# Kernel tuning notes

Measured on AMD Instinct MI355X. Metric: run time of the kernel, lower is better.

Reference implementation:

```python
import jax, jax.numpy as jnp
import numpy as np

P, H, T, B = 16, 24, 168, 4096


def _lstm(x, W_ih, W_hh, b_ih, b_hh):
    # x: [B, T, F]; PyTorch gate order i, f, g, o; returns all hidden states [B, T, H]
    Bsz = x.shape[0]
    Hd = W_hh.shape[1]
    # batch the input GEMM over all timesteps
    xg = jnp.einsum('btf,gf->btg', x, W_ih) + b_ih + b_hh  # [B, T, 4H]

    def step(carry, xt):
        h, c = carry
        g = xt + h @ W_hh.T  # [B, 4H]
        i, f, gg, o = jnp.split(g, 4, axis=-1)
        c = jax.nn.sigmoid(f) * c + jax.nn.sigmoid(i) * jnp.tanh(gg)
        h = jax.nn.sigmoid(o) * jnp.tanh(c)
        return (h, c), h

    h0 = jnp.zeros((Bsz, Hd), x.dtype)
    _, hs = jax.lax.scan(step, (h0, h0), jnp.swapaxes(xg, 0, 1))
    return jnp.swapaxes(hs, 0, 1)  # [B, T, H]


def setup_inputs() -> dict:
    key = jax.random.key(0)
    ks = jax.random.split(key, 14)
    s1 = 1.0 / np.sqrt(H)
    u = lambda k, shape: jax.random.uniform(k, shape, jnp.float32, -s1, s1)
    return {
        'x': jax.random.normal(ks[0], (B, T, P), jnp.float32),
        'W_ih1': u(ks[1], (4 * H, P)), 'W_hh1': u(ks[2], (4 * H, H)),
        'b_ih1': u(ks[3], (4 * H,)), 'b_hh1': u(ks[4], (4 * H,)),
        'W_ih2': u(ks[5], (4 * H, H)), 'W_hh2': u(ks[6], (4 * H, H)),
        'b_ih2': u(ks[7], (4 * H,)), 'b_hh2': u(ks[8], (4 * H,)),
        'W1': u(ks[9], (16, H)), 'b1': u(ks[10], (16,)),
        'W2': u(ks[11], (H, 16)), 'b2': u(ks[12], (H,)),
    }


def reference(x, W_ih1, W_hh1, b_ih1, b_hh1, W_ih2, W_hh2, b_ih2, b_hh2, W1, b1, W2, b2):
    h = jnp.tanh(_lstm(x, W_ih1, W_hh1, b_ih1, b_hh1))       # [B, T, H]
    h = jnp.tanh(_lstm(h, W_ih2, W_hh2, b_ih2, b_hh2))       # [B, T, H]
    h = h[:, -1, :]                                           # [B, H]
    h = jax.nn.relu(h @ W1.T + b1)                            # [B, 16]; dropout = identity (eval mode)
    out = h @ W2.T + b2                                       # [B, 24]
    return out.reshape(out.shape[0], -1, 1)                   # [B, 24, 1]
```

## Files before the change

kernel.cpp:

```cpp
#include <hip/hip_runtime.h>

constexpr int T  = 168;
constexpr int P  = 16;
constexpr int H  = 24;
constexpr int R  = 4;
constexpr int K2 = 24;

__device__ __forceinline__ float rcp_f(float x) { return __builtin_amdgcn_rcpf(x); }
__device__ __forceinline__ float sigm_f(float x) { return rcp_f(1.f + __expf(-x)); }
__device__ __forceinline__ float tanh_fast(float x) {
    return fmaf(2.f, rcp_f(1.f + __expf(-2.f * x)), -1.f);
}
#define LDS_SYNC() asm volatile("s_waitcnt lgkmcnt(0)" ::: "memory")

__global__ __attribute__((amdgpu_flat_work_group_size(128, 128),
                          amdgpu_waves_per_eu(2, 2)))
void lstm2_pipe(const float* __restrict__ x,
                const float* __restrict__ Wih1, const float* __restrict__ Whh1,
                const float* __restrict__ bih1, const float* __restrict__ bhh1,
                const float* __restrict__ Wih2, const float* __restrict__ Whh2,
                const float* __restrict__ bih2, const float* __restrict__ bhh2,
                const float* __restrict__ W1, const float* __restrict__ b1,
                const float* __restrict__ W2, const float* __restrict__ b2,
                float* __restrict__ out)
{
    const int tid  = threadIdx.x;
    const int ph   = tid >> 6;
    const int lane = tid & 63;
    const int s    = (lane < 48) ? lane : 47;
    const int u    = s % H;
    const int half = s / H;
    const int q0   = half * H + u;
    const int q1   = (2 + half) * H + u;
    const int row0 = blockIdx.x * R;

    __shared__ __align__(16) float xbuf[2][R][32];
    __shared__ __align__(16) float t1b [2][R][32];
    __shared__ __align__(16) float t2b [2][R][32];
    __shared__ __align__(16) float h1s [R][32];
    __shared__ __align__(16) float h2s [R][32];
    __shared__ __align__(16) float hd  [R][16];

    float wa0[K2], wa1[K2];
    float wb0[K2], wb1[K2];
    float bi0, bi1;
    if (ph == 0) {
        #pragma unroll
        for (int k = 0; k < P / 4; ++k) {
            float4 a = ((const float4*)(Wih1 + q0 * P))[k];
            float4 b = ((const float4*)(Wih1 + q1 * P))[k];
            wa0[4*k] = a.x; wa0[4*k+1] = a.y; wa0[4*k+2] = a.z; wa0[4*k+3] = a.w;
            wa1[4*k] = b.x; wa1[4*k+1] = b.y; wa1[4*k+2] = b.z; wa1[4*k+3] = b.w;
        }
        #pragma unroll
        for (int k = P; k < K2; ++k) { wa0[k] = 0.f; wa1[k] = 0.f; }
        #pragma unroll
        for (int k = 0; k < H / 4; ++k) {
            float4 a = ((const float4*)(Whh1 + q0 * H))[k];
            float4 b = ((const float4*)(Whh1 + q1 * H))[k];
            wb0[4*k] = a.x; wb0[4*k+1] = a.y; wb0[4*k+2] = a.z; wb0[4*k+3] = a.w;
            wb1[4*k] = b.x; wb1[4*k+1] = b.y; wb1[4*k+2] = b.z; wb1[4*k+3] = b.w;
        }
        bi0 = bih1[q0] + bhh1[q0];
        bi1 = bih1[q1] + bhh1[q1];
    } else {
        #pragma unroll
        for (int k = 0; k < H / 4; ++k) {
            float4 a = ((const float4*)(Wih2 + q0 * H))[k];
            float4 b = ((const float4*)(Wih2 + q1 * H))[k];
            wa0[4*k] = a.x; wa0[4*k+1] = a.y; wa0[4*k+2] = a.z; wa0[4*k+3] = a.w;
            wa1[4*k] = b.x; wa1[4*k+1] = b.y; wa1[4*k+2] = b.z; wa1[4*k+3] = b.w;
        }
        #pragma unroll
        for (int k = 0; k < H / 4; ++k) {
            float4 a = ((const float4*)(Whh2 + q0 * H))[k];
            float4 b = ((const float4*)(Whh2 + q1 * H))[k];
            wb0[4*k] = a.x; wb0[4*k+1] = a.y; wb0[4*k+2] = a.z; wb0[4*k+3] = a.w;
            wb1[4*k] = b.x; wb1[4*k+1] = b.y; wb1[4*k+2] = b.z; wb1[4*k+3] = b.w;
        }
        bi0 = bih2[q0] + bhh2[q0];
        bi1 = bih2[q1] + bhh2[q1];
    }

    if (ph == 0) {
        if (lane < H) {
            #pragma unroll
            for (int r = 0; r < R; ++r) h1s[r][lane] = 0.f;
        }
        for (int f = lane; f < 128; f += 64) {
            int p = f >> 6, rem = f & 63, r = rem >> 4, k = rem & 15;
            xbuf[p][r][16 + k] = 0.f;
        }
        {
            int rr = lane >> 4, kk = lane & 15;
            xbuf[0][rr][kk] = x[(size_t)(row0 + rr) * T * P + kk];
        }
    } else {
        if (lane < H) {
            #pragma unroll
            for (int r = 0; r < R; ++r) h2s[r][lane] = 0.f;
        }
    }
    __syncthreads();

    const float* in1base = (ph == 0) ? &xbuf[0][0][0] : &t1b[0][0][0];
    float*       in2base = (ph == 0) ? &h1s[0][0]     : &h2s[0][0];
    float*       outbase = (ph == 0) ? &t1b[0][0][0]  : &t2b[0][0][0];

    float c[R];
    #pragma unroll
    for (int r = 0; r < R; ++r) c[r] = 0.f;

    for (int i = 0; i <= T; ++i) {
        if ((unsigned)(i - ph) < (unsigned)T) {
            const float* in1 = in1base + (size_t)((i + ph) & 1) * (R * 32);
            float*       tou = outbase + (size_t)(i & 1) * (R * 32);
            #pragma unroll
            for (int r = 0; r < R; ++r) {
                float g0 = bi0, g1 = bi1;
                #pragma unroll
                for (int k = 0; k < K2 / 4; ++k) {
                    float4 a = ((const float4*)(in1 + r * 32))[k];
                    float4 b = ((const float4*)(in2base + r * 32))[k];
                    g0 = fmaf(a.x, wa0[4*k],   g0);  g1 = fmaf(a.x, wa1[4*k],   g1);
                    g0 = fmaf(a.y, wa0[4*k+1], g0);  g1 = fmaf(a.y, wa1[4*k+1], g1);
                    g0 = fmaf(a.z, wa0[4*k+2], g0);  g1 = fmaf(a.z, wa1[4*k+2], g1);
                    g0 = fmaf(a.w, wa0[4*k+3], g0);  g1 = fmaf(a.w, wa1[4*k+3], g1);
                    g0 = fmaf(b.x, wb0[4*k],   g0);  g1 = fmaf(b.x, wb1[4*k],   g1);
                    g0 = fmaf(b.y, wb0[4*k+1], g0);  g1 = fmaf(b.y, wb1[4*k+1], g1);
                    g0 = fmaf(b.z, wb0[4*k+2], g0);  g1 = fmaf(b.z, wb1[4*k+2], g1);
                    g0 = fmaf(b.w, wb0[4*k+3], g0);  g1 = fmaf(b.w, wb1[4*k+3], g1);
                }
                float a0 = sigm_f(g0);
                float px = (half == 0) ? g1 + g1 : g1;
                float sv = sigm_f(px);
                float a1 = (half == 0) ? sv + sv - 1.f : sv;
                float fa = __shfl(a0, lane + 24);
                float oa = __shfl(a1, lane + 24);
                c[r] = fmaf(fa, c[r], a0 * a1);
                float hv = oa * tanh_fast(c[r]);
                float th = tanh_fast(hv);
                if (lane < H) {
                    *(in2base + r * 32 + lane) = hv;
                    *(tou     + r * 32 + lane) = th;
                }
            }
        }
        if (ph == 0 && i + 1 < T) {
            int rr = lane >> 4, kk = lane & 15;
            xbuf[(i + 1) & 1][rr][kk] =
                x[(size_t)(row0 + rr) * T * P + (size_t)(i + 1) * P + kk];
        }
        __syncthreads();
    }

    if (ph == 1) {
        float w1r[H];
        float w2r[16];
        if (lane < 16) {
            #pragma unroll
            for (int j = 0; j < H; ++j) w1r[j] = W1[lane * H + j];
        }
        if (lane < H) {
            #pragma unroll
            for (int j = 0; j < 16; ++j) w2r[j] = W2[lane * 16 + j];
        }
        #pragma unroll
        for (int r = 0; r < R; ++r) {
            if (lane < 16) {
                float acc = b1[lane];
                #pragma unroll
                for (int j = 0; j < H; ++j) acc = fmaf(t2b[0][r][j], w1r[j], acc);
                hd[r][lane] = fmaxf(acc, 0.f);
            }
            LDS_SYNC();
            if (lane < H) {
                float acc = b2[lane];
                #pragma unroll
                for (int j = 0; j < 16; ++j) acc = fmaf(hd[r][j], w2r[j], acc);
                out[(size_t)(row0 + r) * H + lane] = acc;
            }
            LDS_SYNC();
        }
    }
}

extern "C" void kernel_launch(void* const* d_in, const int* in_sizes, int n_in,
                              void* d_out, int out_size, void* d_ws, size_t ws_size,
                              hipStream_t stream)
{
    const float* x    = (const float*)d_in[0];
    const float* Wih1 = (const float*)d_in[1];
    const float* Whh1 = (const float*)d_in[2];
    const float* bih1 = (const float*)d_in[3];
    const float* bhh1 = (const float*)d_in[4];
    const float* Wih2 = (const float*)d_in[5];
    const float* Whh2 = (const float*)d_in[6];
    const float* bih2 = (const float*)d_in[7];
    const float* bhh2 = (const float*)d_in[8];
    const float* W1   = (const float*)d_in[9];
    const float* b1   = (const float*)d_in[10];
    const float* W2   = (const float*)d_in[11];
    const float* b2   = (const float*)d_in[12];
    float* out = (float*)d_out;

    const int B = in_sizes[0] / (T * P);
    hipLaunchKernelGGL(lstm2_pipe, dim3(B / R), dim3(128), 0, stream,
                       x, Wih1, Whh1, bih1, bhh1, Wih2, Whh2, bih2, bhh2,
                       W1, b1, W2, b2, out);
}
```

Baseline: 438.6 us.

## Broadcast recurrent state via readlane instead of LDS, load x directly from global

The recurrent hidden state now stays in registers, and its elements are broadcast to all lanes with v_readlane (scalar broadcast) instead of a round trip through shared memory. The input x is read straight from global memory each step, replacing the double-buffered LDS staging. Only the layer-1 to layer-2 handoff still goes through LDS. The head MLP also uses readlane broadcasts and no longer needs LDS scratch or waitcnt. The aim is to remove LDS latency from the serial recurrence, at the cost of many readlane instructions and, for x, global load latency with no explicit prefetch on the critical path. The padded zero weights for x (k=16..23) are dropped, which removes useless FMAs.

```diff
diff --git a/kernel.cpp b/kernel.cpp
--- a/kernel.cpp
+++ b/kernel.cpp
@@ -1,28 +1,29 @@
 #include <hip/hip_runtime.h>
 
-constexpr int T  = 168;
-constexpr int P  = 16;
-constexpr int H  = 24;
-constexpr int R  = 4;
-constexpr int K2 = 24;
+constexpr int T = 168;
+constexpr int P = 16;
+constexpr int H = 24;
+constexpr int R = 4;
 
 __device__ __forceinline__ float rcp_f(float x) { return __builtin_amdgcn_rcpf(x); }
 __device__ __forceinline__ float sigm_f(float x) { return rcp_f(1.f + __expf(-x)); }
 __device__ __forceinline__ float tanh_fast(float x) {
     return fmaf(2.f, rcp_f(1.f + __expf(-2.f * x)), -1.f);
 }
-#define LDS_SYNC() asm volatile("s_waitcnt lgkmcnt(0)" ::: "memory")
+__device__ __forceinline__ float bcastl(float v, int l) {
+    return __int_as_float(__builtin_amdgcn_readlane(__float_as_int(v), l));
+}
 
 __global__ __attribute__((amdgpu_flat_work_group_size(128, 128),
                           amdgpu_waves_per_eu(2, 2)))
-void lstm2_pipe(const float* __restrict__ x,
-                const float* __restrict__ Wih1, const float* __restrict__ Whh1,
-                const float* __restrict__ bih1, const float* __restrict__ bhh1,
-                const float* __restrict__ Wih2, const float* __restrict__ Whh2,
-                const float* __restrict__ bih2, const float* __restrict__ bhh2,
-                const float* __restrict__ W1, const float* __restrict__ b1,
-                const float* __restrict__ W2, const float* __restrict__ b2,
-                float* __restrict__ out)
+void lstm2_rl(const float* __restrict__ x,
+              const float* __restrict__ Wih1, const float* __restrict__ Whh1,
+              const float* __restrict__ bih1, const float* __restrict__ bhh1,
+              const float* __restrict__ Wih2, const float* __restrict__ Whh2,
+              const float* __restrict__ bih2, const float* __restrict__ bhh2,
+              const float* __restrict__ W1, const float* __restrict__ b1,
+              const float* __restrict__ W2, const float* __restrict__ b2,
+              float* __restrict__ out)
 {
     const int tid  = threadIdx.x;
     const int ph   = tid >> 6;
@@ -34,153 +35,113 @@
     const int q1   = (2 + half) * H + u;
     const int row0 = blockIdx.x * R;
 
-    __shared__ __align__(16) float xbuf[2][R][32];
-    __shared__ __align__(16) float t1b [2][R][32];
-    __shared__ __align__(16) float t2b [2][R][32];
-    __shared__ __align__(16) float h1s [R][32];
-    __shared__ __align__(16) float h2s [R][32];
-    __shared__ __align__(16) float hd  [R][16];
+    __shared__ __align__(16) float t1b[2][R][32];
 
-    float wa0[K2], wa1[K2];
-    float wb0[K2], wb1[K2];
+    float A0[H], A1[H], B0[H], B1[H];
     float bi0, bi1;
     if (ph == 0) {
         #pragma unroll
-        for (int k = 0; k < P / 4; ++k) {
-            float4 a = ((const float4*)(Wih1 + q0 * P))[k];
-            float4 b = ((const float4*)(Wih1 + q1 * P))[k];
-            wa0[4*k] = a.x; wa0[4*k+1] = a.y; wa0[4*k+2] = a.z; wa0[4*k+3] = a.w;
-            wa1[4*k] = b.x; wa1[4*k+1] = b.y; wa1[4*k+2] = b.z; wa1[4*k+3] = b.w;
-        }
+        for (int k = 0; k < P; ++k) { A0[k] = Wih1[q0 * P + k]; A1[k] = Wih1[q1 * P + k]; }
         #pragma unroll
-        for (int k = P; k < K2; ++k) { wa0[k] = 0.f; wa1[k] = 0.f; }
+        for (int k = P; k < H; ++k) { A0[k] = 0.f; A1[k] = 0.f; }
         #pragma unroll
-        for (int k = 0; k < H / 4; ++k) {
-            float4 a = ((const float4*)(Whh1 + q0 * H))[k];
-            float4 b = ((const float4*)(Whh1 + q1 * H))[k];
-            wb0[4*k] = a.x; wb0[4*k+1] = a.y; wb0[4*k+2] = a.z; wb0[4*k+3] = a.w;
-            wb1[4*k] = b.x; wb1[4*k+1] = b.y; wb1[4*k+2] = b.z; wb1[4*k+3] = b.w;
-        }
+        for (int k = 0; k < H; ++k) { B0[k] = Whh1[q0 * H + k]; B1[k] = Whh1[q1 * H + k]; }
         bi0 = bih1[q0] + bhh1[q0];
         bi1 = bih1[q1] + bhh1[q1];
     } else {
         #pragma unroll
-        for (int k = 0; k < H / 4; ++k) {
-            float4 a = ((const float4*)(Wih2 + q0 * H))[k];
-            float4 b = ((const float4*)(Wih2 + q1 * H))[k];
-            wa0[4*k] = a.x; wa0[4*k+1] = a.y; wa0[4*k+2] = a.z; wa0[4*k+3] = a.w;
-            wa1[4*k] = b.x; wa1[4*k+1] = b.y; wa1[4*k+2] = b.z; wa1[4*k+3] = b.w;
-        }
+        for (int k = 0; k < H; ++k) { A0[k] = Wih2[q0 * H + k]; A1[k] = Wih2[q1 * H + k]; }
         #pragma unroll
-        for (int k = 0; k < H / 4; ++k) {
-            float4 a = ((const float4*)(Whh2 + q0 * H))[k];
-            float4 b = ((const float4*)(Whh2 + q1 * H))[k];
-            wb0[4*k] = a.x; wb0[4*k+1] = a.y; wb0[4*k+2] = a.z; wb0[4*k+3] = a.w;
-            wb1[4*k] = b.x; wb1[4*k+1] = b.y; wb1[4*k+2] = b.z; wb1[4*k+3] = b.w;
-        }
+        for (int k = 0; k < H; ++k) { B0[k] = Whh2[q0 * H + k]; B1[k] = Whh2[q1 * H + k]; }
         bi0 = bih2[q0] + bhh2[q0];
         bi1 = bih2[q1] + bhh2[q1];
     }
 
-    if (ph == 0) {
-        if (lane < H) {
-            #pragma unroll
-            for (int r = 0; r < R; ++r) h1s[r][lane] = 0.f;
-        }
-        for (int f = lane; f < 128; f += 64) {
-            int p = f >> 6, rem = f & 63, r = rem >> 4, k = rem & 15;
-            xbuf[p][r][16 + k] = 0.f;
-        }
-        {
-            int rr = lane >> 4, kk = lane & 15;
-            xbuf[0][rr][kk] = x[(size_t)(row0 + rr) * T * P + kk];
-        }
-    } else {
-        if (lane < H) {
-            #pragma unroll
-            for (int r = 0; r < R; ++r) h2s[r][lane] = 0.f;
-        }
-    }
-    __syncthreads();
-
-    const float* in1base = (ph == 0) ? &xbuf[0][0][0] : &t1b[0][0][0];
-    float*       in2base = (ph == 0) ? &h1s[0][0]     : &h2s[0][0];
-    float*       outbase = (ph == 0) ? &t1b[0][0][0]  : &t2b[0][0][0];
-
-    float c[R];
+    float hA[R], c[R];
     #pragma unroll
-    for (int r = 0; r < R; ++r) c[r] = 0.f;
+    for (int r = 0; r < R; ++r) { hA[r] = 0.f; c[r] = 0.f; }
 
     for (int i = 0; i <= T; ++i) {
-        if ((unsigned)(i - ph) < (unsigned)T) {
-            const float* in1 = in1base + (size_t)((i + ph) & 1) * (R * 32);
-            float*       tou = outbase + (size_t)(i & 1) * (R * 32);
-            #pragma unroll
-            for (int r = 0; r < R; ++r) {
-                float g0 = bi0, g1 = bi1;
+        if (ph == 0) {
+            if (i < T) {
                 #pragma unroll
-                for (int k = 0; k < K2 / 4; ++k) {
-                    float4 a = ((const float4*)(in1 + r * 32))[k];
-                    float4 b = ((const float4*)(in2base + r * 32))[k];
-                    g0 = fmaf(a.x, wa0[4*k],   g0);  g1 = fmaf(a.x, wa1[4*k],   g1);
-                    g0 = fmaf(a.y, wa0[4*k+1], g0);  g1 = fmaf(a.y, wa1[4*k+1], g1);
-                    g0 = fmaf(a.z, wa0[4*k+2], g0);  g1 = fmaf(a.z, wa1[4*k+2], g1);
-                    g0 = fmaf(a.w, wa0[4*k+3], g0);  g1 = fmaf(a.w, wa1[4*k+3], g1);
-                    g0 = fmaf(b.x, wb0[4*k],   g0);  g1 = fmaf(b.x, wb1[4*k],   g1);
-                    g0 = fmaf(b.y, wb0[4*k+1], g0);  g1 = fmaf(b.y, wb1[4*k+1], g1);
-                    g0 = fmaf(b.z, wb0[4*k+2], g0);  g1 = fmaf(b.z, wb1[4*k+2], g1);
-                    g0 = fmaf(b.w, wb0[4*k+3], g0);  g1 = fmaf(b.w, wb1[4*k+3], g1);
-                }
-                float a0 = sigm_f(g0);
-                float px = (half == 0) ? g1 + g1 : g1;
-                float sv = sigm_f(px);
-                float a1 = (half == 0) ? sv + sv - 1.f : sv;
-                float fa = __shfl(a0, lane + 24);
-                float oa = __shfl(a1, lane + 24);
-                c[r] = fmaf(fa, c[r], a0 * a1);
-                float hv = oa * tanh_fast(c[r]);
-                float th = tanh_fast(hv);
-                if (lane < H) {
-                    *(in2base + r * 32 + lane) = hv;
-                    *(tou     + r * 32 + lane) = th;
+                for (int r = 0; r < R; ++r) {
+                    const float* xr = x + ((size_t)(row0 + r) * T + i) * P;
+                    float g0 = bi0, g1 = bi1;
+                    #pragma unroll
+                    for (int k = 0; k < P; ++k) {
+                        float xv = xr[k];
+                        g0 = fmaf(xv, A0[k], g0);
+                        g1 = fmaf(xv, A1[k], g1);
+                    }
+                    #pragma unroll
+                    for (int k = 0; k < H; ++k) {
+                        float hk = bcastl(hA[r], k);
+                        g0 = fmaf(hk, B0[k], g0);
+                        g1 = fmaf(hk, B1[k], g1);
+                    }
+                    float a0 = sigm_f(g0);
+                    float px = (half == 0) ? g1 + g1 : g1;
+                    float sv = sigm_f(px);
+                    float a1 = (half == 0) ? sv + sv - 1.f : sv;
+                    float fa = __shfl(a0, lane + 24);
+                    float oa = __shfl(a1, lane + 24);
+                    c[r] = fmaf(fa, c[r], a0 * a1);
+                    hA[r] = oa * tanh_fast(c[r]);
+                    float th = tanh_fast(hA[r]);
+                    if (lane < H) t1b[i & 1][r][lane] = th;
                 }
             }
-        }
-        if (ph == 0 && i + 1 < T) {
-            int rr = lane >> 4, kk = lane & 15;
-            xbuf[(i + 1) & 1][rr][kk] =
-                x[(size_t)(row0 + rr) * T * P + (size_t)(i + 1) * P + kk];
+        } else {
+            if (i >= 1) {
+                #pragma unroll
+                for (int r = 0; r < R; ++r) {
+                    float tv = t1b[(i + 1) & 1][r][lane & 31];
+                    float g0 = bi0, g1 = bi1;
+                    #pragma unroll
+                    for (int k = 0; k < H; ++k) {
+                        float tk = bcastl(tv, k);
+                        float hk = bcastl(hA[r], k);
+                        g0 = fmaf(tk, A0[k], g0);
+                        g1 = fmaf(tk, A1[k], g1);
+                        g0 = fmaf(hk, B0[k], g0);
+                        g1 = fmaf(hk, B1[k], g1);
+                    }
+                    float a0 = sigm_f(g0);
+                    float px = (half == 0) ? g1 + g1 : g1;
+                    float sv = sigm_f(px);
+                    float a1 = (half == 0) ? sv + sv - 1.f : sv;
+                    float fa = __shfl(a0, lane + 24);
+                    float oa = __shfl(a1, lane + 24);
+                    c[r] = fmaf(fa, c[r], a0 * a1);
+                    hA[r] = oa * tanh_fast(c[r]);
+                }
+            }
         }
         __syncthreads();
     }
 
     if (ph == 1) {
-        float w1r[H];
-        float w2r[16];
-        if (lane < 16) {
-            #pragma unroll
-            for (int j = 0; j < H; ++j) w1r[j] = W1[lane * H + j];
-        }
-        if (lane < H) {
-            #pragma unroll
-            for (int j = 0; j < 16; ++j) w2r[j] = W2[lane * 16 + j];
-        }
+        const int l16 = lane & 15;
+        const int l24 = (lane < H) ? lane : 0;
+        float w1r[H], w2r[16];
+        #pragma unroll
+        for (int j = 0; j < H; ++j)  w1r[j] = W1[l16 * H + j];
+        #pragma unroll
+        for (int j = 0; j < 16; ++j) w2r[j] = W2[l24 * 16 + j];
+        const float b1v = b1[l16];
+        const float b2v = b2[l24];
         #pragma unroll
         for (int r = 0; r < R; ++r) {
-            if (lane < 16) {
-                float acc = b1[lane];
-                #pragma unroll
-                for (int j = 0; j < H; ++j) acc = fmaf(t2b[0][r][j], w1r[j], acc);
-                hd[r][lane] = fmaxf(acc, 0.f);
-            }
-            LDS_SYNC();
-            if (lane < H) {
-                float acc = b2[lane];
-                #pragma unroll
-                for (int j = 0; j < 16; ++j) acc = fmaf(hd[r][j], w2r[j], acc);
-                out[(size_t)(row0 + r) * H + lane] = acc;
-            }
-            LDS_SYNC();
+            float th2 = tanh_fast(hA[r]);
+            float acc1 = b1v;
+            #pragma unroll
+            for (int j = 0; j < H; ++j) acc1 = fmaf(bcastl(th2, j), w1r[j], acc1);
+            acc1 = fmaxf(acc1, 0.f);
+            float acc2 = b2v;
+            #pragma unroll
+            for (int j = 0; j < 16; ++j) acc2 = fmaf(bcastl(acc1, j), w2r[j], acc2);
+            if (lane < H) out[(size_t)(row0 + r) * H + lane] = acc2;
         }
     }
 }
@@ -205,7 +166,7 @@
     float* out = (float*)d_out;
 
     const int B = in_sizes[0] / (T * P);
-    hipLaunchKernelGGL(lstm2_pipe, dim3(B / R), dim3(128), 0, stream,
+    hipLaunchKernelGGL(lstm2_rl, dim3(B / R), dim3(128), 0, stream,
                        x, Wih1, Whh1, bih1, bhh1, Wih2, Whh2, bih2, bhh2,
                        W1, b1, W2, b2, out);
 }
```

New measurement: 685.2 us. 1.56x slower.
